# Kernel optimization log

Hardware: AMD Instinct MI355X
Metric: run time of the kernel (lower is better)

## Reference

```python
import jax, jax.numpy as jnp
import numpy as np

N_TOKEN = 267735
D_PROJ = 1024
CUTOFF_ENDS = [0, 20000, 40000, 200000, 267735]
D_EMBS = [1024, 256, 64, 16]  # d_embed // div_val**i, div_val=4
EMB_SCALE = float(D_PROJ) ** 0.5


def setup_inputs() -> dict:
    key = jax.random.key(0)
    ks = jax.random.split(key, 9)
    inp = jax.random.randint(ks[0], (8, 2048), 0, N_TOKEN)
    d = {"inp": inp}
    for i in range(4):
        size = CUTOFF_ENDS[i + 1] - CUTOFF_ENDS[i]
        de = D_EMBS[i]
        d[f"emb{i}"] = jax.random.normal(ks[1 + 2 * i], (size, de), jnp.float32) * 0.02
        d[f"proj{i}"] = jax.random.normal(ks[2 + 2 * i], (D_PROJ, de), jnp.float32) * 0.02
    return d


def reference(inp, emb0, emb1, emb2, emb3, proj0, proj1, proj2, proj3):
    embs = [emb0, emb1, emb2, emb3]
    projs = [proj0, proj1, proj2, proj3]
    flat = inp.reshape(-1)  # [T]
    out = jnp.zeros((flat.shape[0], D_PROJ), jnp.float32)
    for i in range(4):
        l, r = CUTOFF_ENDS[i], CUTOFF_ENDS[i + 1]
        mask = (flat >= l) & (flat < r)  # clusters are disjoint
        idx = jnp.clip(flat - l, 0, r - l - 1)  # in-range dummy where masked out
        # gather [T, d_emb_i] then project to [T, d_proj] (F.linear with weight [d_proj, d_emb_i])
        e = jnp.einsum('td,pd->tp', embs[i][idx], projs[i])
        out = jnp.where(mask[:, None], e, out)
    return (out * EMB_SCALE).reshape(*inp.shape, D_PROJ)
```

## Files before the change

kernel.cpp:

```cpp
#include <hip/hip_runtime.h>


#define CUT0 20000
#define CUT1 40000
#define CUT2 200000

#define PB1 (1024 * 1024)
#define PB2 (PB1 + 1024 * 256)
#define PB3 (PB2 + 1024 * 64)
#define PBEND (PB3 + 1024 * 32)

typedef __attribute__((ext_vector_type(8))) short bf16x8;
typedef __attribute__((ext_vector_type(8))) unsigned short u16x8;
typedef __attribute__((ext_vector_type(4))) float f32x4;

__device__ __forceinline__ unsigned short f2bf(float f) {
    unsigned u = __float_as_uint(f);
    u += 0x7FFFu + ((u >> 16) & 1u);
    return (unsigned short)(u >> 16);
}

__device__ __forceinline__ u16x8 cvt8(const float* __restrict__ s) {
    float4 a = *(const float4*)s;
    float4 b = *(const float4*)(s + 4);
    return (u16x8){f2bf(a.x), f2bf(a.y), f2bf(a.z), f2bf(a.w),
                   f2bf(b.x), f2bf(b.y), f2bf(b.z), f2bf(b.w)};
}

__device__ __forceinline__ void gl_lds16(const unsigned short* g, unsigned short* s) {
    __builtin_amdgcn_global_load_lds(
        (const __attribute__((address_space(1))) void*)g,
        (__attribute__((address_space(3))) void*)s, 16, 0, 0);
}

__global__ __launch_bounds__(256)
void classify_convert(const int* __restrict__ inp, unsigned* __restrict__ counters,
                      unsigned* __restrict__ lists, int T,
                      const float* __restrict__ proj0, const float* __restrict__ proj1,
                      const float* __restrict__ proj2, const float* __restrict__ proj3,
                      unsigned short* __restrict__ projbf) {
    int t = blockIdx.x * 256 + threadIdx.x;
    int lane = threadIdx.x & 63;
    bool valid = (t < T);
    int id = valid ? inp[t] : 0;
    int c = -1, l = 0;
    if (valid) {
        if (id < CUT0)      { c = 0; l = 0; }
        else if (id < CUT1) { c = 1; l = CUT0; }
        else if (id < CUT2) { c = 2; l = CUT1; }
        else                { c = 3; l = CUT2; }
    }
    #pragma unroll
    for (int i = 0; i < 4; ++i) {
        unsigned long long m = __ballot(c == i);
        if (c == i) {
            int leader = __ffsll(m) - 1;
            unsigned base = 0;
            if (lane == leader) base = atomicAdd(&counters[i], (unsigned)__popcll(m));
            base = __shfl(base, leader);
            unsigned rank = (unsigned)__popcll(m & ((1ull << lane) - 1ull));
            lists[(size_t)i * T + base + rank] = ((unsigned)t << 18) | (unsigned)(id - l);
        }
    }
    const int stride = gridDim.x * 256;
    for (int u = t; u < PBEND / 8; u += stride) {
        int base = u * 8;
        u16x8 o;
        if (base < PB1)       o = cvt8(proj0 + base);
        else if (base < PB2)  o = cvt8(proj1 + (base - PB1));
        else if (base < PB3)  o = cvt8(proj2 + (base - PB2));
        else {
            int rel = base - PB3;
            int row = rel >> 5, col = rel & 31;
            if (col < 16) o = cvt8(proj3 + row * 16 + col);
            else          o = (u16x8){0, 0, 0, 0, 0, 0, 0, 0};
        }
        *(u16x8*)(projbf + base) = o;
    }
}

__global__ __launch_bounds__(256)
void gather_bf16(const float* __restrict__ emb0, const float* __restrict__ emb1,
                 const float* __restrict__ emb2, const float* __restrict__ emb3,
                 const unsigned* __restrict__ lists, const unsigned* __restrict__ counters,
                 int T, unsigned short* __restrict__ ecomp) {
    const int c0 = (int)counters[0], c1 = (int)counters[1];
    const int c2 = (int)counters[2], c3 = (int)counters[3];
    const size_t off1 = (size_t)((c0 + 63) & ~63) * 1024;
    const size_t off2 = off1 + (size_t)((c1 + 63) & ~63) * 256;
    const size_t off3 = off2 + (size_t)((c2 + 63) & ~63) * 64;
    const int n0 = c0 << 7, n1 = c1 << 5, n2 = c2 << 3, n3 = c3 << 2;
    const int total = n0 + n1 + n2 + n3;
    const int stride = gridDim.x * 256;
    for (int u = blockIdx.x * 256 + threadIdx.x; u < total; u += stride) {
        int v = u;
        if (v < n0) {
            int r = v >> 7, j = v & 127;
            unsigned id = lists[r] & 0x3FFFFu;
            *(u16x8*)(ecomp + (size_t)r * 1024 + j * 8) = cvt8(emb0 + (size_t)id * 1024 + j * 8);
        } else if ((v -= n0) < n1) {
            int r = v >> 5, j = v & 31;
            unsigned id = lists[T + r] & 0x3FFFFu;
            *(u16x8*)(ecomp + off1 + (size_t)r * 256 + j * 8) = cvt8(emb1 + (size_t)id * 256 + j * 8);
        } else if ((v -= n1) < n2) {
            int r = v >> 3, j = v & 7;
            unsigned id = lists[2 * T + r] & 0x3FFFFu;
            *(u16x8*)(ecomp + off2 + (size_t)r * 64 + j * 8) = cvt8(emb2 + (size_t)id * 64 + j * 8);
        } else {
            v -= n2;
            int r = v >> 2, j = v & 3;
            unsigned id = lists[3 * T + r] & 0x3FFFFu;
            unsigned short* d = ecomp + off3 + (size_t)r * 32 + j * 8;
            if (j < 2) *(u16x8*)d = cvt8(emb3 + (size_t)id * 16 + j * 8);
            else       *(u16x8*)d = (u16x8){0, 0, 0, 0, 0, 0, 0, 0};
        }
    }
}

template<int KP>
__device__ __forceinline__
void tile_gemm(const unsigned short* __restrict__ E, const unsigned short* __restrict__ P,
               const unsigned* __restrict__ list, int count, int mtile, int ntile,
               float* __restrict__ out,
               unsigned short* E_s, unsigned short* P_s, unsigned* pk_s) {
    constexpr int KB  = (KP >= 64) ? 64 : KP;
    constexpr int NCH = KP / KB;
    constexpr int KST = KB / 32;
    constexpr int CPR = KB / 8;
    constexpr int SWZ = CPR - 1;

    const int m0 = mtile * 64;
    const int rows = min(64, count - m0);
    const int py = ntile * 128;
    const int tid = (int)threadIdx.x;
    const int lane = tid & 63;
    const int w  = tid >> 6;
    const int ln = lane & 15;
    const int qd = lane >> 4;

    if (tid < 64) pk_s[tid] = (tid < rows) ? list[m0 + tid] : 0u;

    f32x4 acc[8];
    #pragma unroll
    for (int ct = 0; ct < 8; ++ct) acc[ct] = (f32x4){0.f, 0.f, 0.f, 0.f};

    const unsigned short* eb = E + (size_t)m0 * KP;
    const unsigned short* pb = P + (size_t)py * KP;

    for (int ch = 0; ch < NCH; ++ch) {
        const int k0 = ch * KB;
        #pragma unroll
        for (int it = 0; it < (64 * CPR) / 256; ++it) {
            int i16 = it * 256 + tid;
            int row = i16 / CPR, cc = (i16 % CPR) ^ (row & SWZ);
            gl_lds16(eb + (size_t)row * KP + k0 + cc * 8, E_s + i16 * 8);
        }
        #pragma unroll
        for (int it = 0; it < (128 * CPR) / 256; ++it) {
            int i16 = it * 256 + tid;
            int row = i16 / CPR, cc = (i16 % CPR) ^ (row & SWZ);
            gl_lds16(pb + (size_t)row * KP + k0 + cc * 8, P_s + i16 * 8);
        }
        __syncthreads();

        const int ar = w * 16 + ln;
        #pragma unroll
        for (int s = 0; s < KST; ++s) {
            bf16x8 a = *(const bf16x8*)(E_s + ar * KB + (((s * 4 + qd) ^ (ar & SWZ)) * 8));
            #pragma unroll
            for (int ct = 0; ct < 8; ++ct) {
                const int br = ct * 16 + ln;
                bf16x8 b = *(const bf16x8*)(P_s + br * KB + (((s * 4 + qd) ^ (br & SWZ)) * 8));
                acc[ct] = __builtin_amdgcn_mfma_f32_16x16x32_bf16(a, b, acc[ct], 0, 0, 0);
            }
        }
        __syncthreads();
    }

    #pragma unroll
    for (int ct = 0; ct < 8; ++ct) {
        #pragma unroll
        for (int r = 0; r < 4; ++r) {
            int row = w * 16 + qd * 4 + r;
            if (row < rows) {
                int t = (int)(pk_s[row] >> 18);
                out[(size_t)t * 1024 + py + ct * 16 + ln] = acc[ct][r] * 32.0f;
            }
        }
    }
    __syncthreads();
}

__global__ __launch_bounds__(256)
void gemm_fused(const unsigned short* __restrict__ ecomp, const unsigned short* __restrict__ projbf,
                const unsigned* __restrict__ lists, const unsigned* __restrict__ counters,
                int T, float* __restrict__ out) {
    __shared__ unsigned short E_s[64 * 64];
    __shared__ unsigned short P_s[128 * 64];
    __shared__ unsigned pk_s[64];

    const int c0 = (int)counters[0], c1 = (int)counters[1];
    const int c2 = (int)counters[2], c3 = (int)counters[3];
    const size_t off1 = (size_t)((c0 + 63) & ~63) * 1024;
    const size_t off2 = off1 + (size_t)((c1 + 63) & ~63) * 256;
    const size_t off3 = off2 + (size_t)((c2 + 63) & ~63) * 64;
    const int g0 = (c0 + 63) >> 6;
    const int g1 = g0 + ((c1 + 63) >> 6);
    const int g2 = g1 + ((c2 + 63) >> 6);
    const int g3 = g2 + ((c3 + 63) >> 6);

    const int xcd = blockIdx.x & 7;
    const int slot = blockIdx.x >> 3;
    const int nslots = gridDim.x >> 3;

    for (int i = slot; ; i += nslots) {
        const int g = ((i >> 3) << 3) + xcd;
        if (g >= g3) break;
        const int nt = i & 7;
        if (g < g0)      tile_gemm<1024>(ecomp,        projbf,       lists,         c0, g,      nt, out, E_s, P_s, pk_s);
        else if (g < g1) tile_gemm< 256>(ecomp + off1, projbf + PB1, lists + T,     c1, g - g0, nt, out, E_s, P_s, pk_s);
        else if (g < g2) tile_gemm<  64>(ecomp + off2, projbf + PB2, lists + 2 * T, c2, g - g1, nt, out, E_s, P_s, pk_s);
        else             tile_gemm<  32>(ecomp + off3, projbf + PB3, lists + 3 * T, c3, g - g2, nt, out, E_s, P_s, pk_s);
    }
}

extern "C" void kernel_launch(void* const* d_in, const int* in_sizes, int n_in,
                              void* d_out, int out_size, void* d_ws, size_t ws_size,
                              hipStream_t stream) {
    const int*   inp   = (const int*)d_in[0];
    const float* emb0  = (const float*)d_in[1];
    const float* proj0 = (const float*)d_in[2];
    const float* emb1  = (const float*)d_in[3];
    const float* proj1 = (const float*)d_in[4];
    const float* emb2  = (const float*)d_in[5];
    const float* proj2 = (const float*)d_in[6];
    const float* emb3  = (const float*)d_in[7];
    const float* proj3 = (const float*)d_in[8];
    float* out = (float*)d_out;
    const int T = in_sizes[0];

    unsigned* counters = (unsigned*)d_ws;
    unsigned* lists    = (unsigned*)((char*)d_ws + 256);
    size_t lists_b = ((size_t)4 * T * 4 + 255) & ~(size_t)255;
    unsigned short* projbf = (unsigned short*)((char*)d_ws + 256 + lists_b);
    unsigned short* ecomp  = projbf + PBEND;

    hipMemsetAsync(counters, 0, 16, stream);
    classify_convert<<<dim3(256), 256, 0, stream>>>(inp, counters, lists, T,
                                                    proj0, proj1, proj2, proj3, projbf);
    gather_bf16<<<dim3(2048), 256, 0, stream>>>(emb0, emb1, emb2, emb3,
                                                lists, counters, T, ecomp);
    gemm_fused<<<dim3(1536), 256, 0, stream>>>(ecomp, projbf, lists, counters, T, out);
}
```

Before: 212.7 us.

## Double-buffer LDS GEMM tiles, use direct-register path for small clusters, retune grids

The LDS-tiled GEMM now double-buffers E and P chunks so the global-to-LDS load of the next K chunk overlaps the MFMA work on the current one. The small-K clusters (64 and 32) skip LDS and barriers entirely and load their MFMA operands straight from global memory into registers. Launch sizes of all three kernels change as well. Doubling LDS per block may reduce occupancy, which the smaller GEMM grid partly reflects.

Result: no change. 215.4 us (+1.2%).

```diff
diff --git a/kernel.cpp b/kernel.cpp
--- a/kernel.cpp
+++ b/kernel.cpp
@@ -117,18 +117,13 @@
     }
 }
 
+
 template<int KP>
 __device__ __forceinline__
-void tile_gemm(const unsigned short* __restrict__ E, const unsigned short* __restrict__ P,
-               const unsigned* __restrict__ list, int count, int mtile, int ntile,
-               float* __restrict__ out,
-               unsigned short* E_s, unsigned short* P_s, unsigned* pk_s) {
-    constexpr int KB  = (KP >= 64) ? 64 : KP;
-    constexpr int NCH = KP / KB;
-    constexpr int KST = KB / 32;
-    constexpr int CPR = KB / 8;
-    constexpr int SWZ = CPR - 1;
-
+void tile_gemm_reg(const unsigned short* __restrict__ E, const unsigned short* __restrict__ P,
+                   const unsigned* __restrict__ list, int count, int mtile, int ntile,
+                   float* __restrict__ out) {
+    constexpr int KST = KP / 32;
     const int m0 = mtile * 64;
     const int rows = min(64, count - m0);
     const int py = ntile * 128;
@@ -138,43 +133,98 @@
     const int ln = lane & 15;
     const int qd = lane >> 4;
 
+    const unsigned short* ea = E + (size_t)(m0 + w * 16 + ln) * KP + qd * 8;
+    const unsigned short* pb = P + (size_t)(py + ln) * KP + qd * 8;
+
+    f32x4 acc[8];
+    #pragma unroll
+    for (int ct = 0; ct < 8; ++ct) acc[ct] = (f32x4){0.f, 0.f, 0.f, 0.f};
+
+    #pragma unroll
+    for (int s = 0; s < KST; ++s) {
+        bf16x8 a = *(const bf16x8*)(ea + s * 32);
+        #pragma unroll
+        for (int ct = 0; ct < 8; ++ct) {
+            bf16x8 b = *(const bf16x8*)(pb + (size_t)ct * 16 * KP + s * 32);
+            acc[ct] = __builtin_amdgcn_mfma_f32_16x16x32_bf16(a, b, acc[ct], 0, 0, 0);
+        }
+    }
+
+    int trow[4];
+    #pragma unroll
+    for (int r = 0; r < 4; ++r) {
+        int row = w * 16 + qd * 4 + r;
+        trow[r] = (row < rows) ? (int)(list[m0 + row] >> 18) : -1;
+    }
+    #pragma unroll
+    for (int ct = 0; ct < 8; ++ct)
+        #pragma unroll
+        for (int r = 0; r < 4; ++r)
+            if (trow[r] >= 0)
+                out[(size_t)trow[r] * 1024 + py + ct * 16 + ln] = acc[ct][r] * 32.0f;
+}
+
+template<int KP>
+__device__ __forceinline__
+void tile_gemm_lds(const unsigned short* __restrict__ E, const unsigned short* __restrict__ P,
+                   const unsigned* __restrict__ list, int count, int mtile, int ntile,
+                   float* __restrict__ out,
+                   unsigned short* E_s, unsigned short* P_s, unsigned* pk_s) {
+    constexpr int NCH = KP / 64;
+    const int m0 = mtile * 64;
+    const int rows = min(64, count - m0);
+    const int py = ntile * 128;
+    const int tid = (int)threadIdx.x;
+    const int lane = tid & 63;
+    const int w  = tid >> 6;
+    const int ln = lane & 15;
+    const int qd = lane >> 4;
+
     if (tid < 64) pk_s[tid] = (tid < rows) ? list[m0 + tid] : 0u;
 
+    const unsigned short* eb = E + (size_t)m0 * KP;
+    const unsigned short* pg = P + (size_t)py * KP;
+
+    auto STAGE = [&](int h, int ch) {
+        const int k0 = ch * 64;
+        #pragma unroll
+        for (int it = 0; it < 2; ++it) {
+            int i16 = it * 256 + tid;
+            int row = i16 >> 3, cc = (i16 & 7) ^ (row & 7);
+            gl_lds16(eb + (size_t)row * KP + k0 + cc * 8, E_s + h * (64 * 64) + i16 * 8);
+        }
+        #pragma unroll
+        for (int it = 0; it < 4; ++it) {
+            int i16 = it * 256 + tid;
+            int row = i16 >> 3, cc = (i16 & 7) ^ (row & 7);
+            gl_lds16(pg + (size_t)row * KP + k0 + cc * 8, P_s + h * (128 * 64) + i16 * 8);
+        }
+    };
+
     f32x4 acc[8];
     #pragma unroll
     for (int ct = 0; ct < 8; ++ct) acc[ct] = (f32x4){0.f, 0.f, 0.f, 0.f};
 
-    const unsigned short* eb = E + (size_t)m0 * KP;
-    const unsigned short* pb = P + (size_t)py * KP;
-
+    STAGE(0, 0);
+    __syncthreads();
+    int cur = 0;
     for (int ch = 0; ch < NCH; ++ch) {
-        const int k0 = ch * KB;
-        #pragma unroll
-        for (int it = 0; it < (64 * CPR) / 256; ++it) {
-            int i16 = it * 256 + tid;
-            int row = i16 / CPR, cc = (i16 % CPR) ^ (row & SWZ);
-            gl_lds16(eb + (size_t)row * KP + k0 + cc * 8, E_s + i16 * 8);
-        }
-        #pragma unroll
-        for (int it = 0; it < (128 * CPR) / 256; ++it) {
-            int i16 = it * 256 + tid;
-            int row = i16 / CPR, cc = (i16 % CPR) ^ (row & SWZ);
-            gl_lds16(pb + (size_t)row * KP + k0 + cc * 8, P_s + i16 * 8);
-        }
-        __syncthreads();
-
+        if (ch + 1 < NCH) STAGE(cur ^ 1, ch + 1);
+        const unsigned short* Eb = E_s + cur * (64 * 64);
+        const unsigned short* Pb = P_s + cur * (128 * 64);
         const int ar = w * 16 + ln;
         #pragma unroll
-        for (int s = 0; s < KST; ++s) {
-            bf16x8 a = *(const bf16x8*)(E_s + ar * KB + (((s * 4 + qd) ^ (ar & SWZ)) * 8));
+        for (int s = 0; s < 2; ++s) {
+            bf16x8 a = *(const bf16x8*)(Eb + ar * 64 + (((s * 4 + qd) ^ (ar & 7)) * 8));
             #pragma unroll
             for (int ct = 0; ct < 8; ++ct) {
                 const int br = ct * 16 + ln;
-                bf16x8 b = *(const bf16x8*)(P_s + br * KB + (((s * 4 + qd) ^ (br & SWZ)) * 8));
+                bf16x8 b = *(const bf16x8*)(Pb + br * 64 + (((s * 4 + qd) ^ (br & 7)) * 8));
                 acc[ct] = __builtin_amdgcn_mfma_f32_16x16x32_bf16(a, b, acc[ct], 0, 0, 0);
             }
         }
         __syncthreads();
+        cur ^= 1;
     }
 
     #pragma unroll
@@ -195,8 +245,8 @@
 void gemm_fused(const unsigned short* __restrict__ ecomp, const unsigned short* __restrict__ projbf,
                 const unsigned* __restrict__ lists, const unsigned* __restrict__ counters,
                 int T, float* __restrict__ out) {
-    __shared__ unsigned short E_s[64 * 64];
-    __shared__ unsigned short P_s[128 * 64];
+    __shared__ unsigned short E_s[2 * 64 * 64];
+    __shared__ unsigned short P_s[2 * 128 * 64];
     __shared__ unsigned pk_s[64];
 
     const int c0 = (int)counters[0], c1 = (int)counters[1];
@@ -217,10 +267,10 @@
         const int g = ((i >> 3) << 3) + xcd;
         if (g >= g3) break;
         const int nt = i & 7;
-        if (g < g0)      tile_gemm<1024>(ecomp,        projbf,       lists,         c0, g,      nt, out, E_s, P_s, pk_s);
-        else if (g < g1) tile_gemm< 256>(ecomp + off1, projbf + PB1, lists + T,     c1, g - g0, nt, out, E_s, P_s, pk_s);
-        else if (g < g2) tile_gemm<  64>(ecomp + off2, projbf + PB2, lists + 2 * T, c2, g - g1, nt, out, E_s, P_s, pk_s);
-        else             tile_gemm<  32>(ecomp + off3, projbf + PB3, lists + 3 * T, c3, g - g2, nt, out, E_s, P_s, pk_s);
+        if (g < g0)      tile_gemm_lds<1024>(ecomp,        projbf,       lists,         c0, g,      nt, out, E_s, P_s, pk_s);
+        else if (g < g1) tile_gemm_lds< 256>(ecomp + off1, projbf + PB1, lists + T,     c1, g - g0, nt, out, E_s, P_s, pk_s);
+        else if (g < g2) tile_gemm_reg<  64>(ecomp + off2, projbf + PB2, lists + 2 * T, c2, g - g1, nt, out);
+        else             tile_gemm_reg<  32>(ecomp + off3, projbf + PB3, lists + 3 * T, c3, g - g2, nt, out);
     }
 }
 
@@ -246,9 +296,9 @@
     unsigned short* ecomp  = projbf + PBEND;
 
     hipMemsetAsync(counters, 0, 16, stream);
-    classify_convert<<<dim3(256), 256, 0, stream>>>(inp, counters, lists, T,
+    classify_convert<<<dim3(512), 256, 0, stream>>>(inp, counters, lists, T,
                                                     proj0, proj1, proj2, proj3, projbf);
-    gather_bf16<<<dim3(2048), 256, 0, stream>>>(emb0, emb1, emb2, emb3,
+    gather_bf16<<<dim3(1024), 256, 0, stream>>>(emb0, emb1, emb2, emb3,
                                                 lists, counters, T, ecomp);
-    gemm_fused<<<dim3(1536), 256, 0, stream>>>(ecomp, projbf, lists, counters, T, out);
-}
+    gemm_fused<<<dim3(768), 256, 0, stream>>>(ecomp, projbf, lists, counters, T, out);
+}
```
